# Kernel tuning notes

Measured on AMD Instinct MI355X. Metric: run time of the kernel, lower is better.

## Reference

```python
import jax, jax.numpy as jnp
import numpy as np

NUM_GROUPS = 4
NUM_HEADS = 4
EPS = 1e-6

def group_norm(x, scale, bias):
    # x: [B, C, L]
    b, c, l = x.shape
    g = NUM_GROUPS
    xg = x.reshape(b, g, (c // g) * l)
    mean = xg.mean(axis=-1, keepdims=True)
    var = xg.var(axis=-1, keepdims=True)
    xg = (xg - mean) * jax.lax.rsqrt(var + EPS)
    xn = xg.reshape(b, c, l)
    return xn * scale[None, :, None] + bias[None, :, None]

def conv1x1(x, w, b):
    # x: [B, C_in, L], w: [C_out, C_in], b: [C_out]
    return jnp.einsum('oc,bcl->bol', w, x) + b[None, :, None]

def setup_inputs() -> dict:
    key = jax.random.key(0)
    ks = jax.random.split(key, 11)
    B, C, L = 8, 512, 2048
    x = jax.random.normal(ks[0], (B, C, L), dtype=jnp.float32)
    s = 1.0 / np.sqrt(C)
    return {
        'x': x,
        'gn_scale': jnp.ones((C,), jnp.float32),
        'gn_bias': jnp.zeros((C,), jnp.float32),
        'wq': jax.random.normal(ks[1], (C, C), jnp.float32) * s,
        'bq': jnp.zeros((C,), jnp.float32),
        'wk': jax.random.normal(ks[2], (C, C), jnp.float32) * s,
        'bk': jnp.zeros((C,), jnp.float32),
        'wv': jax.random.normal(ks[3], (C, C), jnp.float32) * s,
        'bv': jnp.zeros((C,), jnp.float32),
        'wo': jax.random.normal(ks[4], (C, C), jnp.float32) * s,
        'bo': jnp.zeros((C,), jnp.float32),
    }

def reference(x, gn_scale, gn_bias, wq, bq, wk, bk, wv, bv, wo, bo):
    b, c, l = x.shape
    nh = NUM_HEADS
    hd = c // nh
    h_ = group_norm(x, gn_scale, gn_bias)
    q = conv1x1(h_, wq, bq).reshape(b, nh, hd, l)
    k = conv1x1(h_, wk, bk).reshape(b, nh, hd, l)
    v = conv1x1(h_, wv, bv).reshape(b, nh, hd, l)
    # scores: [b, nh, l(query), l(key)]
    w_ = jnp.einsum('bhdq,bhdk->bhqk', q, k) * (hd ** -0.5)
    w_ = jax.nn.softmax(w_, axis=-1)
    # attn: [b, nh, l(query), hd]
    attn = jnp.einsum('bhqk,bhdk->bhqd', w_, v)
    attn = attn.transpose(0, 1, 3, 2).reshape(b, c, l)
    out = conv1x1(attn, wo, bo)
    return x + out
```

## Files before the change

### kernel.cpp

```cpp
#include <hip/hip_runtime.h>


typedef unsigned short u16;
typedef unsigned int   u32;
typedef unsigned long long u64;
typedef __attribute__((ext_vector_type(8)))  short          bf16x8;
typedef __attribute__((ext_vector_type(4)))  float          f32x4;
typedef __attribute__((ext_vector_type(4)))  unsigned int   u32x4;
typedef __attribute__((ext_vector_type(8)))  unsigned short u16x8;

#define MFMA16(a, b, c) __builtin_amdgcn_mfma_f32_16x16x32_bf16((a), (b), (c), 0, 0, 0)

#define WAIT_VM12        3964
#define WAIT_VM8_LGKM0    120
#define BARRIER() __builtin_amdgcn_s_barrier()

__device__ __forceinline__ u16 f2bf(float f) {
    union { float f; unsigned int i; } cv;
    cv.f = f;
    unsigned int u = cv.i;
    u += 0x7fffu + ((u >> 16) & 1);
    return (u16)(u >> 16);
}
__device__ __forceinline__ u32 fbits(float f) {
    union { float f; unsigned int i; } cv; cv.f = f; return cv.i;
}

__device__ __forceinline__ void async16(const u16* g, u16* l) {
    __builtin_amdgcn_global_load_lds(
        (const __attribute__((address_space(1))) unsigned int*)g,
        (__attribute__((address_space(3))) unsigned int*)l, 16, 0, 0);
}

#define BATCH 8
#define CCH   512
#define LEN   2048
#define NGRP  4
#define NHEAD 4
#define HD    128
#define GSIZE (128 * 2048)

__global__ __launch_bounds__(256) void wcvt_k(const float* __restrict__ w0,
                                              const float* __restrict__ w1,
                                              const float* __restrict__ w2,
                                              const float* __restrict__ w3,
                                              u16* __restrict__ dst) {
    const int mat = blockIdx.y;
    const float* src = (mat == 0) ? w0 : (mat == 1) ? w1 : (mat == 2) ? w2 : w3;
    const size_t base = (size_t)blockIdx.x * 2048 + (size_t)threadIdx.x * 8;
    f32x4 a = *(const f32x4*)(src + base);
    f32x4 b = *(const f32x4*)(src + base + 4);
    u16x8 o;
    for (int u = 0; u < 4; ++u) { o[u] = f2bf(a[u]); o[u + 4] = f2bf(b[u]); }
    *(u16x8*)(dst + (size_t)mat * 262144 + base) = o;
}

__global__ __launch_bounds__(256) void gn_stats_k(const float* __restrict__ x,
                                                  float* __restrict__ stats) {
    const int bid   = blockIdx.x;
    const int grp   = bid >> 3;
    const int chunk = bid & 7;
    const int b = grp >> 2, g = grp & 3;
    const float* base = x + ((size_t)(b * CCH + g * 128 + chunk * 16)) * LEN;

    float s = 0.f, ss = 0.f;
    for (int i = 0; i < 32; ++i) {
        int cid = threadIdx.x + i * 256;
        f32x4 dv = *(const f32x4*)(base + (size_t)cid * 4);
        for (int u = 0; u < 4; ++u) { s += dv[u]; ss += dv[u] * dv[u]; }
    }
    for (int m = 1; m < 64; m <<= 1) {
        s  += __shfl_xor(s,  m, 64);
        ss += __shfl_xor(ss, m, 64);
    }
    __shared__ float red[8];
    int wid = threadIdx.x >> 6, lane = threadIdx.x & 63;
    if (lane == 0) { red[wid * 2] = s; red[wid * 2 + 1] = ss; }
    __syncthreads();
    if (threadIdx.x == 0) {
        float ts  = red[0] + red[2] + red[4] + red[6];
        float tss = red[1] + red[3] + red[5] + red[7];
        atomicAdd(&stats[grp * 2],     ts);
        atomicAdd(&stats[grp * 2 + 1], tss);
    }
}

__global__ __launch_bounds__(256) void gn_apply_k(const float* __restrict__ x,
                                                  const float* __restrict__ gns,
                                                  const float* __restrict__ gnb,
                                                  const float* __restrict__ stats,
                                                  u16* __restrict__ hT) {
    __shared__ u16 Ts[64 * 72];
    const int b = blockIdx.z, c0 = blockIdx.y * 64, l0 = blockIdx.x * 64;
    const int g = c0 >> 7;
    const int tid = threadIdx.x;

    float sum   = stats[(b * NGRP + g) * 2];
    float sumsq = stats[(b * NGRP + g) * 2 + 1];
    const float invN = 1.f / (float)GSIZE;
    float mean = sum * invN;
    float var  = sumsq * invN - mean * mean;
    float rstd = rsqrtf(var + 1e-6f);

    for (int i = 0; i < 4; ++i) {
        int cid = tid + i * 256;
        int row = cid >> 4, c4 = cid & 15;
        int c = c0 + row;
        float sc = gns[c] * rstd;
        float bi = gnb[c] - mean * sc;
        f32x4 dv = *(const f32x4*)(x + ((size_t)(b * CCH + c)) * LEN + l0 + c4 * 4);
        for (int u = 0; u < 4; ++u)
            Ts[row * 72 + c4 * 4 + u] = f2bf(dv[u] * sc + bi);
    }
    __syncthreads();
    for (int i = 0; i < 2; ++i) {
        int cid = tid + i * 256;
        int lrow = cid >> 3, c8 = cid & 7;
        u16x8 ov;
        for (int u = 0; u < 8; ++u) ov[u] = Ts[(c8 * 8 + u) * 72 + lrow];
        *(u16x8*)(hT + ((size_t)b * LEN + l0 + lrow) * CCH + c0 + c8 * 8) = ov;
    }
}

template <int MODE>
__global__ __launch_bounds__(256, 2) void gemm_k(const u16* __restrict__ A0,
                                                 const u16* __restrict__ B0,
                                                 const u16* __restrict__ B1,
                                                 const float* __restrict__ bias0,
                                                 const float* __restrict__ bias1,
                                                 const float* __restrict__ resid,
                                                 void* __restrict__ out0v,
                                                 u16* __restrict__ out1) {
    __shared__ u16 As[2][128 * 64];
    __shared__ u16 Bs[2][128 * 64];
    const int b  = blockIdx.z;
    const int n0 = blockIdx.x * 128;
    const int m0 = blockIdx.y * 128;
    const int tid = threadIdx.x;
    const int lane = tid & 63, wid = tid >> 6;
    const int quad = lane >> 4, l15 = lane & 15;
    const int wm = (wid & 1) * 64, wn = (wid >> 1) * 64;

    const u16* Arow;
    if constexpr (MODE == 0) Arow = A0 + ((size_t)b * LEN + m0) * 512;
    else                     Arow = A0 + (size_t)m0 * 512;

    const u16* Brow;
    int col0 = 0;
    if constexpr (MODE == 0) {
        if (n0 < 512) { Brow = B0 + (size_t)n0 * 512;         col0 = n0; }
        else          { Brow = B1 + (size_t)(n0 - 512) * 512;  col0 = n0 - 512; }
    } else {
        Brow = B0 + ((size_t)b * LEN + n0) * 512;
    }

    f32x4 acc[4][4] = {};
    const int srl = lane >> 3, scl = lane & 7;

#pragma unroll
    for (int i = 0; i < 4; ++i) {
        int rloc = wid * 32 + i * 8 + srl;
        int lc = scl ^ (rloc & 7);
        async16(Arow + (size_t)rloc * 512 + lc * 8, &As[0][(wid * 32 + i * 8) * 64]);
        async16(Brow + (size_t)rloc * 512 + lc * 8, &Bs[0][(wid * 32 + i * 8) * 64]);
    }
    __syncthreads();

    for (int kk = 0; kk < 8; ++kk) {
        const int p = kk & 1;
        if (kk < 7) {
            const int k0n = (kk + 1) * 64;
#pragma unroll
            for (int i = 0; i < 4; ++i) {
                int rloc = wid * 32 + i * 8 + srl;
                int lc = scl ^ (rloc & 7);
                async16(Arow + (size_t)rloc * 512 + k0n + lc * 8,
                        &As[1 - p][(wid * 32 + i * 8) * 64]);
                async16(Brow + (size_t)rloc * 512 + k0n + lc * 8,
                        &Bs[1 - p][(wid * 32 + i * 8) * 64]);
            }
        }
#pragma unroll
        for (int ks = 0; ks < 2; ++ks) {
            bf16x8 af[4], bfr[4];
            for (int t = 0; t < 4; ++t) {
                int ra = wm + t * 16 + l15, rb = wn + t * 16 + l15;
                af[t]  = *(const bf16x8*)(&As[p][ra * 64 + (((ks * 4 + quad) ^ (ra & 7))) * 8]);
                bfr[t] = *(const bf16x8*)(&Bs[p][rb * 64 + (((ks * 4 + quad) ^ (rb & 7))) * 8]);
            }
            for (int mt = 0; mt < 4; ++mt)
                for (int nt = 0; nt < 4; ++nt)
                    acc[mt][nt] = MFMA16(af[mt], bfr[nt], acc[mt][nt]);
        }
        __syncthreads();
    }

    if constexpr (MODE == 0) {
        const float* biasp = (n0 < 512) ? (bias0 + col0) : (bias1 + col0);
        u16* outp = (n0 < 512) ? (u16*)out0v : out1;
        for (int nt = 0; nt < 4; ++nt) {
            int nl = wn + nt * 16 + l15;
            float bv_ = biasp[nl];
            for (int mt = 0; mt < 4; ++mt)
                for (int r = 0; r < 4; ++r) {
                    int ml = wm + mt * 16 + quad * 4 + r;
                    size_t idx = ((size_t)b * LEN + m0 + ml) * 512 + col0 + nl;
                    outp[idx] = f2bf(acc[mt][nt][r] + bv_);
                }
        }
    } else {
        for (int mt = 0; mt < 4; ++mt)
            for (int r = 0; r < 4; ++r) {
                int ml = wm + mt * 16 + quad * 4 + r;
                float bv_ = bias0[m0 + ml];
                for (int nt = 0; nt < 4; ++nt) {
                    int nl = wn + nt * 16 + l15;
                    size_t idx = ((size_t)(b * 512 + m0 + ml)) * LEN + n0 + nl;
                    float val = acc[mt][nt][r] + bv_;
                    if constexpr (MODE == 2) {
                        ((float*)out0v)[idx] = val + resid[idx];
                    } else {
                        ((u16*)out0v)[idx] = f2bf(val);
                    }
                }
            }
    }
}

__global__ __launch_bounds__(256, 2) void attn_k(const u16* __restrict__ qT,
                                                 const u16* __restrict__ kT,
                                                 const u16* __restrict__ v,
                                                 u16* __restrict__ attnT) {
    __shared__ u16 Ks[2][64 * 128];
    __shared__ u16 Vs[2][128 * 64];
    const int b = blockIdx.z, h = blockIdx.y;
    const int i0 = blockIdx.x * 128;
    const int tid = threadIdx.x, lane = tid & 63, wid = tid >> 6;
    const int quad = lane >> 4, l15 = lane & 15;

    bf16x8 qa[2][4];
    for (int mf = 0; mf < 2; ++mf)
        for (int ks = 0; ks < 4; ++ks) {
            int m = i0 + wid * 32 + mf * 16 + l15;
            qa[mf][ks] = *(const bf16x8*)(qT + ((size_t)b * LEN + m) * 512 + h * HD +
                                          ks * 32 + quad * 8);
        }

    float mst[2] = {-3.0e38f, -3.0e38f}, lst[2] = {0.f, 0.f};
    f32x4 oacc[2][8] = {};

    const float SL2E = 0.08838834764831845f * 1.4426950408889634f;

    const int srwK = lane >> 4, scK = lane & 15;
    const int srwV = lane >> 3, scV = lane & 7;
    const u16* kbase = kT + ((size_t)b * LEN) * 512 + h * HD;
    const u16* vbase = v + ((size_t)(b * CCH + h * HD)) * LEN;

    const u16* kgp[4];
    const u16* vgp[4];
    int krow[4], vrow[4];
#pragma unroll
    for (int i = 0; i < 4; ++i) {
        int rk = wid * 16 + i * 4 + srwK;
        krow[i] = wid * 16 + i * 4;
        kgp[i] = kbase + (size_t)rk * 512 + (scK ^ (rk & 7)) * 8;
        int rv = wid * 32 + i * 8 + srwV;
        vrow[i] = wid * 32 + i * 8;
        vgp[i] = vbase + (size_t)rv * LEN + (scV ^ (rv & 7)) * 8;
    }

#pragma unroll
    for (int i = 0; i < 4; ++i) {
        async16(kgp[i], &Ks[0][krow[i] * 128]);
        async16(vgp[i], &Vs[0][vrow[i] * 64]);
        kgp[i] += 64 * 512;
        vgp[i] += 64;
    }

    for (int jt = 0; jt < 32; ++jt) {
        const int p = jt & 1;

#pragma unroll
        for (int i = 0; i < 4; ++i) {
            async16(kgp[i], &Ks[1 - p][krow[i] * 128]);
            async16(vgp[i], &Vs[1 - p][vrow[i] * 64]);
        }
        if (jt < 30) {
#pragma unroll
            for (int i = 0; i < 4; ++i) { kgp[i] += 64 * 512; vgp[i] += 64; }
        }

        __builtin_amdgcn_s_waitcnt(WAIT_VM12);
        BARRIER();

        f32x4 st[2][4] = {};
#pragma unroll
        for (int jtn = 0; jtn < 4; ++jtn) {
            int r = jtn * 16 + l15;
            for (int ks = 0; ks < 4; ++ks) {
                bf16x8 kf = *(const bf16x8*)(&Ks[p][r * 128 + ((ks * 4 + quad) ^ (r & 7)) * 8]);
                st[0][jtn] = MFMA16(kf, qa[0][ks], st[0][jtn]);
                st[1][jtn] = MFMA16(kf, qa[1][ks], st[1][jtn]);
            }
        }

        float alpha2[2];
#pragma unroll
        for (int mf = 0; mf < 2; ++mf) {
            float rm = -3.0e38f;
            for (int jtn = 0; jtn < 4; ++jtn)
                for (int r = 0; r < 4; ++r) rm = fmaxf(rm, st[mf][jtn][r]);
            rm *= SL2E;
            rm = fmaxf(rm, __shfl_xor(rm, 16, 64));
            rm = fmaxf(rm, __shfl_xor(rm, 32, 64));
            float mnew  = fmaxf(mst[mf], rm);
            float alpha = __builtin_amdgcn_exp2f(mst[mf] - mnew);
            mst[mf] = mnew;
            float rs = 0.f;
            for (int jtn = 0; jtn < 4; ++jtn)
                for (int r = 0; r < 4; ++r) {
                    float pv_ = __builtin_amdgcn_exp2f(st[mf][jtn][r] * SL2E - mnew);
                    st[mf][jtn][r] = pv_;
                    rs += pv_;
                }
            rs += __shfl_xor(rs, 16, 64);
            rs += __shfl_xor(rs, 32, 64);
            lst[mf] = lst[mf] * alpha + rs;
            alpha2[mf] = alpha;
        }
        if (__ballot(alpha2[0] != 1.0f || alpha2[1] != 1.0f) != 0ull) {
#pragma unroll
            for (int mf = 0; mf < 2; ++mf) {
                float av[4];
                for (int r = 0; r < 4; ++r) av[r] = __shfl(alpha2[mf], quad * 4 + r, 16);
                for (int dt = 0; dt < 8; ++dt)
                    for (int r = 0; r < 4; ++r) oacc[mf][dt][r] *= av[r];
            }
        }

        __builtin_amdgcn_s_waitcnt(WAIT_VM8_LGKM0);
        BARRIER();

#pragma unroll
        for (int mf = 0; mf < 2; ++mf) {
            int m = wid * 32 + mf * 16 + l15;
            for (int jtn = 0; jtn < 4; ++jtn) {
                u64 packed =  (u64)((fbits(st[mf][jtn][0]) + 0x8000u) >> 16)
                           | ((u64)((fbits(st[mf][jtn][1]) + 0x8000u) >> 16) << 16)
                           | ((u64)((fbits(st[mf][jtn][2]) + 0x8000u) >> 16) << 32)
                           | ((u64)((fbits(st[mf][jtn][3]) + 0x8000u) >> 16) << 48);
                int pc = (jtn * 2 + (quad >> 1)) ^ (m & 7);
                *(u64*)(&Ks[p][m * 64 + pc * 8 + (quad & 1) * 4]) = packed;
            }
        }

#pragma unroll
        for (int ks = 0; ks < 2; ++ks) {
            bf16x8 pf[2];
            for (int mf = 0; mf < 2; ++mf) {
                int m = wid * 32 + mf * 16 + l15;
                pf[mf] = *(const bf16x8*)(&Ks[p][m * 64 + ((ks * 4 + quad) ^ (m & 7)) * 8]);
            }
            for (int dt = 0; dt < 8; ++dt) {
                int d = dt * 16 + l15;
                bf16x8 vf = *(const bf16x8*)(&Vs[p][d * 64 + ((ks * 4 + quad) ^ (d & 7)) * 8]);
                oacc[0][dt] = MFMA16(pf[0], vf, oacc[0][dt]);
                oacc[1][dt] = MFMA16(pf[1], vf, oacc[1][dt]);
            }
        }

        __builtin_amdgcn_s_waitcnt(WAIT_VM8_LGKM0);
        BARRIER();
    }

    for (int mf = 0; mf < 2; ++mf) {
        float inv = 1.f / lst[mf];
        float iv[4];
        for (int r = 0; r < 4; ++r) iv[r] = __shfl(inv, quad * 4 + r, 16);
        for (int r = 0; r < 4; ++r) {
            int m = i0 + wid * 32 + mf * 16 + quad * 4 + r;
            for (int dt = 0; dt < 8; ++dt) {
                int d = dt * 16 + l15;
                attnT[((size_t)b * LEN + m) * 512 + h * HD + d] =
                    f2bf(oacc[mf][dt][r] * iv[r]);
            }
        }
    }
}

extern "C" void kernel_launch(void* const* d_in, const int* in_sizes, int n_in,
                              void* d_out, int out_size, void* d_ws, size_t ws_size,
                              hipStream_t stream) {
    const float* x   = (const float*)d_in[0];
    const float* gns = (const float*)d_in[1];
    const float* gnb = (const float*)d_in[2];
    const float* wq  = (const float*)d_in[3];
    const float* bq  = (const float*)d_in[4];
    const float* wk  = (const float*)d_in[5];
    const float* bk  = (const float*)d_in[6];
    const float* wv  = (const float*)d_in[7];
    const float* bv  = (const float*)d_in[8];
    const float* wo  = (const float*)d_in[9];
    const float* bo  = (const float*)d_in[10];
    float* out = (float*)d_out;

    const size_t NEL = (size_t)BATCH * CCH * LEN;
    float* stats = (float*)d_ws;
    u16* wcat  = (u16*)((char*)d_ws + 256);
    u16* hT    = wcat + 4 * 262144;
    u16* qT    = hT + NEL;
    u16* kT    = qT + NEL;
    u16* vbuf  = kT + NEL;
    u16* attnT = hT;

    const u16* wq_bf = wcat;
    const u16* wk_bf = wcat + 262144;
    const u16* wv_bf = wcat + 2 * 262144;
    const u16* wo_bf = wcat + 3 * 262144;

    hipMemsetAsync(d_ws, 0, 256, stream);
    wcvt_k<<<dim3(128, 4), 256, 0, stream>>>(wq, wk, wv, wo, wcat);
    gn_stats_k<<<256, 256, 0, stream>>>(x, stats);
    gn_apply_k<<<dim3(32, 8, 8), 256, 0, stream>>>(x, gns, gnb, stats, hT);
    gemm_k<0><<<dim3(8, 16, 8), 256, 0, stream>>>(hT, wq_bf, wk_bf, bq, bk, nullptr, qT, kT);
    gemm_k<1><<<dim3(16, 4, 8), 256, 0, stream>>>(wv_bf, hT, nullptr, bv, nullptr, nullptr, vbuf, nullptr);
    attn_k<<<dim3(16, 4, 8), 256, 0, stream>>>(qT, kT, vbuf, attnT);
    gemm_k<2><<<dim3(16, 4, 8), 256, 0, stream>>>(wo_bf, attnT, nullptr, bo, nullptr, x, out, nullptr);
}
```

Before: 275.3 us.

## Split attention block work across eight waves with sixteen query rows each

```diff
diff --git a/kernel.cpp b/kernel.cpp
--- a/kernel.cpp
+++ b/kernel.cpp
@@ -11,8 +11,8 @@
 
 #define MFMA16(a, b, c) __builtin_amdgcn_mfma_f32_16x16x32_bf16((a), (b), (c), 0, 0, 0)
 
-#define WAIT_VM12        3964
-#define WAIT_VM8_LGKM0    120
+#define WAIT_VM6         3958
+#define WAIT_VM4_LGKM0    116
 #define BARRIER() __builtin_amdgcn_s_barrier()
 
 __device__ __forceinline__ u16 f2bf(float f) {
@@ -227,7 +227,7 @@
     }
 }
 
-__global__ __launch_bounds__(256, 2) void attn_k(const u16* __restrict__ qT,
+__global__ __launch_bounds__(512, 4) void attn_k(const u16* __restrict__ qT,
                                                  const u16* __restrict__ kT,
                                                  const u16* __restrict__ v,
                                                  u16* __restrict__ attnT) {
@@ -237,40 +237,36 @@
     const int i0 = blockIdx.x * 128;
     const int tid = threadIdx.x, lane = tid & 63, wid = tid >> 6;
     const int quad = lane >> 4, l15 = lane & 15;
-
-    bf16x8 qa[2][4];
-    for (int mf = 0; mf < 2; ++mf)
-        for (int ks = 0; ks < 4; ++ks) {
-            int m = i0 + wid * 32 + mf * 16 + l15;
-            qa[mf][ks] = *(const bf16x8*)(qT + ((size_t)b * LEN + m) * 512 + h * HD +
-                                          ks * 32 + quad * 8);
-        }
-
-    float mst[2] = {-3.0e38f, -3.0e38f}, lst[2] = {0.f, 0.f};
-    f32x4 oacc[2][8] = {};
+    const int mrow = wid * 16 + l15;
+
+    bf16x8 qa[4];
+    for (int ks = 0; ks < 4; ++ks)
+        qa[ks] = *(const bf16x8*)(qT + ((size_t)b * LEN + i0 + mrow) * 512 + h * HD +
+                                  ks * 32 + quad * 8);
+
+    float mst = -3.0e38f, lst = 0.f;
+    f32x4 oacc[8] = {};
 
     const float SL2E = 0.08838834764831845f * 1.4426950408889634f;
 
-    const int srwK = lane >> 4, scK = lane & 15;
-    const int srwV = lane >> 3, scV = lane & 7;
     const u16* kbase = kT + ((size_t)b * LEN) * 512 + h * HD;
     const u16* vbase = v + ((size_t)(b * CCH + h * HD)) * LEN;
 
-    const u16* kgp[4];
-    const u16* vgp[4];
-    int krow[4], vrow[4];
-#pragma unroll
-    for (int i = 0; i < 4; ++i) {
-        int rk = wid * 16 + i * 4 + srwK;
-        krow[i] = wid * 16 + i * 4;
-        kgp[i] = kbase + (size_t)rk * 512 + (scK ^ (rk & 7)) * 8;
-        int rv = wid * 32 + i * 8 + srwV;
-        vrow[i] = wid * 32 + i * 8;
-        vgp[i] = vbase + (size_t)rv * LEN + (scV ^ (rv & 7)) * 8;
-    }
-
-#pragma unroll
-    for (int i = 0; i < 4; ++i) {
+    const u16* kgp[2];
+    const u16* vgp[2];
+    int krow[2], vrow[2];
+#pragma unroll
+    for (int i = 0; i < 2; ++i) {
+        int rk = wid * 8 + i * 4 + (lane >> 4);
+        krow[i] = wid * 8 + i * 4;
+        kgp[i] = kbase + (size_t)rk * 512 + ((lane & 15) ^ (rk & 7)) * 8;
+        int rv = wid * 16 + i * 8 + (lane >> 3);
+        vrow[i] = wid * 16 + i * 8;
+        vgp[i] = vbase + (size_t)rv * LEN + ((lane & 7) ^ (rv & 7)) * 8;
+    }
+
+#pragma unroll
+    for (int i = 0; i < 2; ++i) {
         async16(kgp[i], &Ks[0][krow[i] * 128]);
         async16(vgp[i], &Vs[0][vrow[i] * 64]);
         kgp[i] += 64 * 512;
@@ -281,74 +277,66 @@
         const int p = jt & 1;
 
 #pragma unroll
-        for (int i = 0; i < 4; ++i) {
+        for (int i = 0; i < 2; ++i) {
             async16(kgp[i], &Ks[1 - p][krow[i] * 128]);
             async16(vgp[i], &Vs[1 - p][vrow[i] * 64]);
         }
         if (jt < 30) {
 #pragma unroll
-            for (int i = 0; i < 4; ++i) { kgp[i] += 64 * 512; vgp[i] += 64; }
-        }
-
-        __builtin_amdgcn_s_waitcnt(WAIT_VM12);
+            for (int i = 0; i < 2; ++i) { kgp[i] += 64 * 512; vgp[i] += 64; }
+        }
+
+        __builtin_amdgcn_s_waitcnt(WAIT_VM6);
         BARRIER();
 
-        f32x4 st[2][4] = {};
+        f32x4 st[4] = {};
 #pragma unroll
         for (int jtn = 0; jtn < 4; ++jtn) {
             int r = jtn * 16 + l15;
             for (int ks = 0; ks < 4; ++ks) {
                 bf16x8 kf = *(const bf16x8*)(&Ks[p][r * 128 + ((ks * 4 + quad) ^ (r & 7)) * 8]);
-                st[0][jtn] = MFMA16(kf, qa[0][ks], st[0][jtn]);
-                st[1][jtn] = MFMA16(kf, qa[1][ks], st[1][jtn]);
-            }
-        }
-
-        float alpha2[2];
-#pragma unroll
-        for (int mf = 0; mf < 2; ++mf) {
-            float rm = -3.0e38f;
-            for (int jtn = 0; jtn < 4; ++jtn)
-                for (int r = 0; r < 4; ++r) rm = fmaxf(rm, st[mf][jtn][r]);
-            rm *= SL2E;
-            rm = fmaxf(rm, __shfl_xor(rm, 16, 64));
-            rm = fmaxf(rm, __shfl_xor(rm, 32, 64));
-            float mnew  = fmaxf(mst[mf], rm);
-            float alpha = __builtin_amdgcn_exp2f(mst[mf] - mnew);
-            mst[mf] = mnew;
-            float rs = 0.f;
-            for (int jtn = 0; jtn < 4; ++jtn)
-                for (int r = 0; r < 4; ++r) {
-                    float pv_ = __builtin_amdgcn_exp2f(st[mf][jtn][r] * SL2E - mnew);
-                    st[mf][jtn][r] = pv_;
-                    rs += pv_;
-                }
-            rs += __shfl_xor(rs, 16, 64);
-            rs += __shfl_xor(rs, 32, 64);
-            lst[mf] = lst[mf] * alpha + rs;
-            alpha2[mf] = alpha;
-        }
-        if (__ballot(alpha2[0] != 1.0f || alpha2[1] != 1.0f) != 0ull) {
-#pragma unroll
-            for (int mf = 0; mf < 2; ++mf) {
-                float av[4];
-                for (int r = 0; r < 4; ++r) av[r] = __shfl(alpha2[mf], quad * 4 + r, 16);
-                for (int dt = 0; dt < 8; ++dt)
-                    for (int r = 0; r < 4; ++r) oacc[mf][dt][r] *= av[r];
-            }
-        }
-
-        __builtin_amdgcn_s_waitcnt(WAIT_VM8_LGKM0);
+                st[jtn] = MFMA16(kf, qa[ks], st[jtn]);
+            }
+        }
+
+        float rm = -3.0e38f;
+        for (int jtn = 0; jtn < 4; ++jtn)
+            for (int r = 0; r < 4; ++r) rm = fmaxf(rm, st[jtn][r]);
+        rm *= SL2E;
+        rm = fmaxf(rm, __shfl_xor(rm, 16, 64));
+        rm = fmaxf(rm, __shfl_xor(rm, 32, 64));
+        float mnew  = fmaxf(mst, rm);
+        float alpha = __builtin_amdgcn_exp2f(mst - mnew);
+        mst = mnew;
+        float rs = 0.f;
+        for (int jtn = 0; jtn < 4; ++jtn)
+            for (int r = 0; r < 4; ++r) {
+                float pv_ = __builtin_amdgcn_exp2f(st[jtn][r] * SL2E - mnew);
+                st[jtn][r] = pv_;
+                rs += pv_;
+            }
+        rs += __shfl_xor(rs, 16, 64);
+        rs += __shfl_xor(rs, 32, 64);
+        lst = lst * alpha + rs;
+
+        if (__ballot(alpha != 1.0f) != 0ull) {
+            float av[4];
+            for (int r = 0; r < 4; ++r) av[r] = __shfl(alpha, quad * 4 + r, 16);
+            for (int dt = 0; dt < 8; ++dt)
+                for (int r = 0; r < 4; ++r) oacc[dt][r] *= av[r];
+        }
+
+        __builtin_amdgcn_s_waitcnt(WAIT_VM4_LGKM0);
         BARRIER();
 
-#pragma unroll
-        for (int mf = 0; mf < 2; ++mf) {
-            int m = wid * 32 + mf * 16 + l15;
+        {
+            int m = mrow;
+#pragma unroll
             for (int jtn = 0; jtn < 4; ++jtn) {
-                u64 packed =  (u64)((fbits(st[mf][jtn][0]) + 0x8000u) >> 16)
-                           | ((u64)((fbits(st[mf][jtn][1]) + 0x8000u) >> 16) << 16)
-                           | ((u64)((fbits(st[mf][jtn][2]) + 0x8000u) >> 16) << 32)
-                           | ((u64)((fbits(st[mf][jtn][3]) + 0x8000u) >> 16) << 48);
+                u64 packed =  (u64)((fbits(st[jtn][0]) + 0x8000u) >> 16)
+                           | ((u64)((fbits(st[jtn][1]) + 0x8000u) >> 16) << 16)
+                           | ((u64)((fbits(st[jtn][2]) + 0x8000u) >> 16) << 32)
+                           | ((u64)((fbits(st[jtn][3]) + 0x8000u) >> 16) << 48);
                 int pc = (jtn * 2 + (quad >> 1)) ^ (m & 7);
                 *(u64*)(&Ks[p][m * 64 + pc * 8 + (quad & 1) * 4]) = packed;
             }
@@ -356,34 +344,26 @@
 
 #pragma unroll
         for (int ks = 0; ks < 2; ++ks) {
-            bf16x8 pf[2];
-            for (int mf = 0; mf < 2; ++mf) {
-                int m = wid * 32 + mf * 16 + l15;
-                pf[mf] = *(const bf16x8*)(&Ks[p][m * 64 + ((ks * 4 + quad) ^ (m & 7)) * 8]);
-            }
+            bf16x8 pf = *(const bf16x8*)(&Ks[p][mrow * 64 + ((ks * 4 + quad) ^ (mrow & 7)) * 8]);
             for (int dt = 0; dt < 8; ++dt) {
                 int d = dt * 16 + l15;
                 bf16x8 vf = *(const bf16x8*)(&Vs[p][d * 64 + ((ks * 4 + quad) ^ (d & 7)) * 8]);
-                oacc[0][dt] = MFMA16(pf[0], vf, oacc[0][dt]);
-                oacc[1][dt] = MFMA16(pf[1], vf, oacc[1][dt]);
-            }
-        }
-
-        __builtin_amdgcn_s_waitcnt(WAIT_VM8_LGKM0);
+                oacc[dt] = MFMA16(pf, vf, oacc[dt]);
+            }
+        }
+
+        __builtin_amdgcn_s_waitcnt(WAIT_VM4_LGKM0);
         BARRIER();
     }
 
-    for (int mf = 0; mf < 2; ++mf) {
-        float inv = 1.f / lst[mf];
-        float iv[4];
-        for (int r = 0; r < 4; ++r) iv[r] = __shfl(inv, quad * 4 + r, 16);
-        for (int r = 0; r < 4; ++r) {
-            int m = i0 + wid * 32 + mf * 16 + quad * 4 + r;
-            for (int dt = 0; dt < 8; ++dt) {
-                int d = dt * 16 + l15;
-                attnT[((size_t)b * LEN + m) * 512 + h * HD + d] =
-                    f2bf(oacc[mf][dt][r] * iv[r]);
-            }
+    float inv = 1.f / lst;
+    float iv[4];
+    for (int r = 0; r < 4; ++r) iv[r] = __shfl(inv, quad * 4 + r, 16);
+    for (int r = 0; r < 4; ++r) {
+        int m = i0 + wid * 16 + quad * 4 + r;
+        for (int dt = 0; dt < 8; ++dt) {
+            int d = dt * 16 + l15;
+            attnT[((size_t)b * LEN + m) * 512 + h * HD + d] = f2bf(oacc[dt][r] * iv[r]);
         }
     }
 }
@@ -424,6 +404,6 @@
     gn_apply_k<<<dim3(32, 8, 8), 256, 0, stream>>>(x, gns, gnb, stats, hT);
     gemm_k<0><<<dim3(8, 16, 8), 256, 0, stream>>>(hT, wq_bf, wk_bf, bq, bk, nullptr, qT, kT);
     gemm_k<1><<<dim3(16, 4, 8), 256, 0, stream>>>(wv_bf, hT, nullptr, bv, nullptr, nullptr, vbuf, nullptr);
-    attn_k<<<dim3(16, 4, 8), 256, 0, stream>>>(qT, kT, vbuf, attnT);
+    attn_k<<<dim3(16, 4, 8), 512, 0, stream>>>(qT, kT, vbuf, attnT);
     gemm_k<2><<<dim3(16, 4, 8), 256, 0, stream>>>(wo_bf, attnT, nullptr, bo, nullptr, x, out, nullptr);
 }
```

After: 271.7 us. No clear change (-1.3%).

## Warp-specialize attention into score and PV waves with cross-iteration pipelining

Applied to the files above, without the earlier changes.

```diff
diff --git a/kernel.cpp b/kernel.cpp
--- a/kernel.cpp
+++ b/kernel.cpp
@@ -11,8 +11,10 @@
 
 #define MFMA16(a, b, c) __builtin_amdgcn_mfma_f32_16x16x32_bf16((a), (b), (c), 0, 0, 0)
 
-#define WAIT_VM12        3964
-#define WAIT_VM8_LGKM0    120
+#define WAIT_VM4       3956
+#define WAIT_VM2       3954
+#define WAIT_LGKM0    49279
+#define WAIT_VM0_LGKM0  112
 #define BARRIER() __builtin_amdgcn_s_barrier()
 
 __device__ __forceinline__ u16 f2bf(float f) {
@@ -227,162 +229,182 @@
     }
 }
 
-__global__ __launch_bounds__(256, 2) void attn_k(const u16* __restrict__ qT,
+__global__ __launch_bounds__(256, 3) void attn_k(const u16* __restrict__ qT,
                                                  const u16* __restrict__ kT,
                                                  const u16* __restrict__ v,
                                                  u16* __restrict__ attnT) {
-    __shared__ u16 Ks[2][64 * 128];
-    __shared__ u16 Vs[2][128 * 64];
-    const int b = blockIdx.z, h = blockIdx.y;
-    const int i0 = blockIdx.x * 128;
+    __shared__ u16  Ks[2][32 * 128];
+    __shared__ u16  Vs[2][128 * 32];
+    __shared__ u16  Ps[2][2][32 * 32];
+    __shared__ float Al[2][2][32];
+    __shared__ float Lf[2][32];
+    const int bid = blockIdx.x;
+    const int xcd = bid & 7, slot = bid >> 3;
+    const int bh  = xcd * 4 + (slot >> 5);
+    const int qt  = slot & 31;
+    const int b = bh >> 2, h = bh & 3;
+    const int i0 = qt * 64;
+
     const int tid = threadIdx.x, lane = tid & 63, wid = tid >> 6;
     const int quad = lane >> 4, l15 = lane & 15;
+    const bool isS = (wid < 2);
+    const int mg = wid & 1;
+
+    const float SL2E = 0.08838834764831845f * 1.4426950408889634f;
+
+    const u16* kbase = kT + ((size_t)b * LEN) * 512 + h * HD;
+    const u16* vbase = v + ((size_t)(b * CCH + h * HD)) * LEN;
+    const u16* kp[2];
+    const u16* vp[2];
+    int krow[2], vrow[2];
+#pragma unroll
+    for (int i = 0; i < 2; ++i) {
+        int rk = (wid * 2 + i) * 4 + (lane >> 4);
+        krow[i] = (wid * 2 + i) * 4;
+        kp[i] = kbase + (size_t)rk * 512 + ((lane & 15) ^ (rk & 7)) * 8;
+        int rd = (wid * 2 + i) * 16 + (lane >> 2);
+        vrow[i] = (wid * 2 + i) * 16;
+        vp[i] = vbase + (size_t)rd * LEN + ((lane & 3) ^ (rd & 3)) * 8;
+    }
 
     bf16x8 qa[2][4];
-    for (int mf = 0; mf < 2; ++mf)
-        for (int ks = 0; ks < 4; ++ks) {
-            int m = i0 + wid * 32 + mf * 16 + l15;
-            qa[mf][ks] = *(const bf16x8*)(qT + ((size_t)b * LEN + m) * 512 + h * HD +
-                                          ks * 32 + quad * 8);
-        }
-
+    if (isS) {
+        for (int mf = 0; mf < 2; ++mf)
+            for (int ks = 0; ks < 4; ++ks) {
+                int m = i0 + mg * 32 + mf * 16 + l15;
+                qa[mf][ks] = *(const bf16x8*)(qT + ((size_t)b * LEN + m) * 512 + h * HD +
+                                              ks * 32 + quad * 8);
+            }
+    }
     float mst[2] = {-3.0e38f, -3.0e38f}, lst[2] = {0.f, 0.f};
     f32x4 oacc[2][8] = {};
 
-    const float SL2E = 0.08838834764831845f * 1.4426950408889634f;
-
-    const int srwK = lane >> 4, scK = lane & 15;
-    const int srwV = lane >> 3, scV = lane & 7;
-    const u16* kbase = kT + ((size_t)b * LEN) * 512 + h * HD;
-    const u16* vbase = v + ((size_t)(b * CCH + h * HD)) * LEN;
-
-    const u16* kgp[4];
-    const u16* vgp[4];
-    int krow[4], vrow[4];
-#pragma unroll
-    for (int i = 0; i < 4; ++i) {
-        int rk = wid * 16 + i * 4 + srwK;
-        krow[i] = wid * 16 + i * 4;
-        kgp[i] = kbase + (size_t)rk * 512 + (scK ^ (rk & 7)) * 8;
-        int rv = wid * 32 + i * 8 + srwV;
-        vrow[i] = wid * 32 + i * 8;
-        vgp[i] = vbase + (size_t)rv * LEN + (scV ^ (rv & 7)) * 8;
-    }
-
-#pragma unroll
-    for (int i = 0; i < 4; ++i) {
-        async16(kgp[i], &Ks[0][krow[i] * 128]);
-        async16(vgp[i], &Vs[0][vrow[i] * 64]);
-        kgp[i] += 64 * 512;
-        vgp[i] += 64;
-    }
-
-    for (int jt = 0; jt < 32; ++jt) {
-        const int p = jt & 1;
-
-#pragma unroll
-        for (int i = 0; i < 4; ++i) {
-            async16(kgp[i], &Ks[1 - p][krow[i] * 128]);
-            async16(vgp[i], &Vs[1 - p][vrow[i] * 64]);
-        }
-        if (jt < 30) {
-#pragma unroll
-            for (int i = 0; i < 4; ++i) { kgp[i] += 64 * 512; vgp[i] += 64; }
-        }
-
-        __builtin_amdgcn_s_waitcnt(WAIT_VM12);
+#pragma unroll
+    for (int i = 0; i < 2; ++i) { async16(kp[i], &Ks[0][krow[i] * 128]); kp[i] += 32 * 512; }
+
+    for (int t = 0; t < 64; ++t) {
+        const int p = t & 1;
+#pragma unroll
+        for (int i = 0; i < 2; ++i) { async16(vp[i], &Vs[p][vrow[i] * 32]); vp[i] += 32; }
+        if (t < 63) {
+#pragma unroll
+            for (int i = 0; i < 2; ++i) {
+                async16(kp[i], &Ks[1 - p][krow[i] * 128]);
+                if (t < 62) kp[i] += 32 * 512;
+            }
+            __builtin_amdgcn_s_waitcnt(WAIT_VM4);
+        } else {
+            __builtin_amdgcn_s_waitcnt(WAIT_VM2);
+        }
         BARRIER();
 
-        f32x4 st[2][4] = {};
-#pragma unroll
-        for (int jtn = 0; jtn < 4; ++jtn) {
-            int r = jtn * 16 + l15;
-            for (int ks = 0; ks < 4; ++ks) {
-                bf16x8 kf = *(const bf16x8*)(&Ks[p][r * 128 + ((ks * 4 + quad) ^ (r & 7)) * 8]);
-                st[0][jtn] = MFMA16(kf, qa[0][ks], st[0][jtn]);
-                st[1][jtn] = MFMA16(kf, qa[1][ks], st[1][jtn]);
-            }
-        }
-
-        float alpha2[2];
-#pragma unroll
-        for (int mf = 0; mf < 2; ++mf) {
-            float rm = -3.0e38f;
-            for (int jtn = 0; jtn < 4; ++jtn)
-                for (int r = 0; r < 4; ++r) rm = fmaxf(rm, st[mf][jtn][r]);
-            rm *= SL2E;
-            rm = fmaxf(rm, __shfl_xor(rm, 16, 64));
-            rm = fmaxf(rm, __shfl_xor(rm, 32, 64));
-            float mnew  = fmaxf(mst[mf], rm);
-            float alpha = __builtin_amdgcn_exp2f(mst[mf] - mnew);
-            mst[mf] = mnew;
-            float rs = 0.f;
-            for (int jtn = 0; jtn < 4; ++jtn)
-                for (int r = 0; r < 4; ++r) {
-                    float pv_ = __builtin_amdgcn_exp2f(st[mf][jtn][r] * SL2E - mnew);
-                    st[mf][jtn][r] = pv_;
-                    rs += pv_;
+        if (isS) {
+            f32x4 st[2][2] = {};
+#pragma unroll
+            for (int jtn = 0; jtn < 2; ++jtn) {
+                int r = jtn * 16 + l15;
+                for (int ks = 0; ks < 4; ++ks) {
+                    bf16x8 kf = *(const bf16x8*)(&Ks[p][r * 128 + ((ks * 4 + quad) ^ (r & 7)) * 8]);
+                    st[0][jtn] = MFMA16(kf, qa[0][ks], st[0][jtn]);
+                    st[1][jtn] = MFMA16(kf, qa[1][ks], st[1][jtn]);
                 }
-            rs += __shfl_xor(rs, 16, 64);
-            rs += __shfl_xor(rs, 32, 64);
-            lst[mf] = lst[mf] * alpha + rs;
-            alpha2[mf] = alpha;
-        }
-        if (__ballot(alpha2[0] != 1.0f || alpha2[1] != 1.0f) != 0ull) {
+            }
 #pragma unroll
             for (int mf = 0; mf < 2; ++mf) {
-                float av[4];
-                for (int r = 0; r < 4; ++r) av[r] = __shfl(alpha2[mf], quad * 4 + r, 16);
-                for (int dt = 0; dt < 8; ++dt)
-                    for (int r = 0; r < 4; ++r) oacc[mf][dt][r] *= av[r];
-            }
-        }
-
-        __builtin_amdgcn_s_waitcnt(WAIT_VM8_LGKM0);
-        BARRIER();
-
-#pragma unroll
-        for (int mf = 0; mf < 2; ++mf) {
-            int m = wid * 32 + mf * 16 + l15;
-            for (int jtn = 0; jtn < 4; ++jtn) {
-                u64 packed =  (u64)((fbits(st[mf][jtn][0]) + 0x8000u) >> 16)
-                           | ((u64)((fbits(st[mf][jtn][1]) + 0x8000u) >> 16) << 16)
-                           | ((u64)((fbits(st[mf][jtn][2]) + 0x8000u) >> 16) << 32)
-                           | ((u64)((fbits(st[mf][jtn][3]) + 0x8000u) >> 16) << 48);
-                int pc = (jtn * 2 + (quad >> 1)) ^ (m & 7);
-                *(u64*)(&Ks[p][m * 64 + pc * 8 + (quad & 1) * 4]) = packed;
-            }
-        }
-
-#pragma unroll
-        for (int ks = 0; ks < 2; ++ks) {
+                float rm = -3.0e38f;
+                for (int jtn = 0; jtn < 2; ++jtn)
+                    for (int r = 0; r < 4; ++r) rm = fmaxf(rm, st[mf][jtn][r]);
+                rm *= SL2E;
+                rm = fmaxf(rm, __shfl_xor(rm, 16, 64));
+                rm = fmaxf(rm, __shfl_xor(rm, 32, 64));
+                float mnew  = fmaxf(mst[mf], rm);
+                float alpha = __builtin_amdgcn_exp2f(mst[mf] - mnew);
+                mst[mf] = mnew;
+                float rs = 0.f;
+                for (int jtn = 0; jtn < 2; ++jtn)
+                    for (int r = 0; r < 4; ++r) {
+                        float pv_ = __builtin_amdgcn_exp2f(st[mf][jtn][r] * SL2E - mnew);
+                        st[mf][jtn][r] = pv_;
+                        rs += pv_;
+                    }
+                rs += __shfl_xor(rs, 16, 64);
+                rs += __shfl_xor(rs, 32, 64);
+                lst[mf] = lst[mf] * alpha + rs;
+                if (quad == 0) Al[p][mg][mf * 16 + l15] = alpha;
+                int ml = mf * 16 + l15;
+                for (int jtn = 0; jtn < 2; ++jtn) {
+                    u64 packed =  (u64)((fbits(st[mf][jtn][0]) + 0x8000u) >> 16)
+                               | ((u64)((fbits(st[mf][jtn][1]) + 0x8000u) >> 16) << 16)
+                               | ((u64)((fbits(st[mf][jtn][2]) + 0x8000u) >> 16) << 32)
+                               | ((u64)((fbits(st[mf][jtn][3]) + 0x8000u) >> 16) << 48);
+                    int pc = (jtn * 2 + (quad >> 1)) ^ (ml & 3);
+                    *(u64*)(&Ps[p][mg][ml * 32 + pc * 8 + (quad & 1) * 4]) = packed;
+                }
+            }
+        } else if (t > 0) {
+            f32x4 av[2];
+            for (int mf = 0; mf < 2; ++mf)
+                av[mf] = *(const f32x4*)(&Al[1 - p][mg][mf * 16 + quad * 4]);
+            bool resc = (av[0][0] != 1.f) || (av[0][1] != 1.f) || (av[0][2] != 1.f) ||
+                        (av[0][3] != 1.f) || (av[1][0] != 1.f) || (av[1][1] != 1.f) ||
+                        (av[1][2] != 1.f) || (av[1][3] != 1.f);
+            if (__ballot(resc) != 0ull) {
+                for (int mf = 0; mf < 2; ++mf)
+                    for (int dt = 0; dt < 8; ++dt)
+                        for (int r = 0; r < 4; ++r) oacc[mf][dt][r] *= av[mf][r];
+            }
             bf16x8 pf[2];
             for (int mf = 0; mf < 2; ++mf) {
-                int m = wid * 32 + mf * 16 + l15;
-                pf[mf] = *(const bf16x8*)(&Ks[p][m * 64 + ((ks * 4 + quad) ^ (m & 7)) * 8]);
+                int ml = mf * 16 + l15;
+                pf[mf] = *(const bf16x8*)(&Ps[1 - p][mg][ml * 32 + (quad ^ (ml & 3)) * 8]);
             }
             for (int dt = 0; dt < 8; ++dt) {
                 int d = dt * 16 + l15;
-                bf16x8 vf = *(const bf16x8*)(&Vs[p][d * 64 + ((ks * 4 + quad) ^ (d & 7)) * 8]);
+                bf16x8 vf = *(const bf16x8*)(&Vs[1 - p][d * 32 + (quad ^ (d & 3)) * 8]);
                 oacc[0][dt] = MFMA16(pf[0], vf, oacc[0][dt]);
                 oacc[1][dt] = MFMA16(pf[1], vf, oacc[1][dt]);
             }
         }
 
-        __builtin_amdgcn_s_waitcnt(WAIT_VM8_LGKM0);
+        __builtin_amdgcn_s_waitcnt(WAIT_LGKM0);
         BARRIER();
     }
 
-    for (int mf = 0; mf < 2; ++mf) {
-        float inv = 1.f / lst[mf];
-        float iv[4];
-        for (int r = 0; r < 4; ++r) iv[r] = __shfl(inv, quad * 4 + r, 16);
-        for (int r = 0; r < 4; ++r) {
-            int m = i0 + wid * 32 + mf * 16 + quad * 4 + r;
-            for (int dt = 0; dt < 8; ++dt) {
-                int d = dt * 16 + l15;
-                attnT[((size_t)b * LEN + m) * 512 + h * HD + d] =
-                    f2bf(oacc[mf][dt][r] * iv[r]);
+    if (isS && quad == 0) {
+        Lf[mg][l15]      = lst[0];
+        Lf[mg][16 + l15] = lst[1];
+    }
+    __builtin_amdgcn_s_waitcnt(WAIT_VM0_LGKM0);
+    BARRIER();
+
+    if (!isS) {
+        f32x4 av[2];
+        for (int mf = 0; mf < 2; ++mf)
+            av[mf] = *(const f32x4*)(&Al[1][mg][mf * 16 + quad * 4]);
+        for (int mf = 0; mf < 2; ++mf)
+            for (int dt = 0; dt < 8; ++dt)
+                for (int r = 0; r < 4; ++r) oacc[mf][dt][r] *= av[mf][r];
+        bf16x8 pf[2];
+        for (int mf = 0; mf < 2; ++mf) {
+            int ml = mf * 16 + l15;
+            pf[mf] = *(const bf16x8*)(&Ps[1][mg][ml * 32 + (quad ^ (ml & 3)) * 8]);
+        }
+        for (int dt = 0; dt < 8; ++dt) {
+            int d = dt * 16 + l15;
+            bf16x8 vf = *(const bf16x8*)(&Vs[1][d * 32 + (quad ^ (d & 3)) * 8]);
+            oacc[0][dt] = MFMA16(pf[0], vf, oacc[0][dt]);
+            oacc[1][dt] = MFMA16(pf[1], vf, oacc[1][dt]);
+        }
+        for (int mf = 0; mf < 2; ++mf) {
+            f32x4 lf = *(const f32x4*)(&Lf[mg][mf * 16 + quad * 4]);
+            for (int r = 0; r < 4; ++r) {
+                float inv = 1.f / lf[r];
+                int m = i0 + mg * 32 + mf * 16 + quad * 4 + r;
+                for (int dt = 0; dt < 8; ++dt) {
+                    int d = dt * 16 + l15;
+                    attnT[((size_t)b * LEN + m) * 512 + h * HD + d] =
+                        f2bf(oacc[mf][dt][r] * inv);
+                }
             }
         }
     }
@@ -424,6 +446,6 @@
     gn_apply_k<<<dim3(32, 8, 8), 256, 0, stream>>>(x, gns, gnb, stats, hT);
     gemm_k<0><<<dim3(8, 16, 8), 256, 0, stream>>>(hT, wq_bf, wk_bf, bq, bk, nullptr, qT, kT);
     gemm_k<1><<<dim3(16, 4, 8), 256, 0, stream>>>(wv_bf, hT, nullptr, bv, nullptr, nullptr, vbuf, nullptr);
-    attn_k<<<dim3(16, 4, 8), 256, 0, stream>>>(qT, kT, vbuf, attnT);
+    attn_k<<<dim3(1024), 256, 0, stream>>>(qT, kT, vbuf, attnT);
     gemm_k<2><<<dim3(16, 4, 8), 256, 0, stream>>>(wo_bf, attnT, nullptr, bo, nullptr, x, out, nullptr);
 }
```

Measured after the change: 349.3 us. 26.9% more time.
